# Kernel tuning notes

Measured on AMD Instinct MI355X. Metric: run time of the kernel, lower is better.

Reference implementation:

```python
import jax, jax.numpy as jnp
import numpy as np

NDIV = (10, 10)
OUT_CHANNEL = 100


def setup_inputs() -> dict:
    key = jax.random.key(0)
    k1, k2 = jax.random.split(key)
    x1 = jax.random.normal(k1, (8, 64, 128, 128), dtype=jnp.float32)
    x2 = jax.random.normal(k2, (8, 64, 60, 60), dtype=jnp.float32)
    return {"x1": x1, "x2": x2}


def reference(x1, x2):
    B, C, H, W = x1.shape
    h, w = x2.shape[-2], x2.shape[-1]
    nd0, nd1 = NDIV
    hh, ww = h // nd0, w // nd1  # patch size (6, 6)
    P = nd0 * nd1                # 100 patches per sample

    # channel-wise L2 normalization (dim=1)
    x1n = x1 / jnp.linalg.norm(x1, axis=1, keepdims=True)
    x2n = x2 / jnp.linalg.norm(x2, axis=1, keepdims=True)

    # extract nd0*nd1 patches per sample as conv filters: [B*P, C, hh, ww]
    patches = x2n.reshape(B, C, nd0, hh, nd1, ww)
    patches = patches.transpose(0, 2, 4, 1, 3, 5).reshape(B * P, C, hh, ww)

    # grouped cross-correlation (torch F.conv2d = correlation, no kernel flip)
    lhs = x1n.reshape(1, B * C, H, W)
    mm = jax.lax.conv_general_dilated(
        lhs, patches,
        window_strides=(1, 1),
        padding=((hh // 2, hh // 2), (ww // 2, ww // 2)),
        feature_group_count=B,
        dimension_numbers=("NCHW", "OIHW", "NCHW"),
    ) / (hh * ww)  # [1, B*P, H+1, W+1] for even hh,ww

    # bilinear resize to (H, W)  (torch align_corners=False == half-pixel)
    mm = jax.image.resize(mm, (1, B * P, H, W), method="bilinear")

    # [B, P, H, W] -> topk over patch dim, then mean
    mm = mm.reshape(B, P, H, W)
    topv = jax.lax.top_k(jnp.moveaxis(mm, 1, -1), OUT_CHANNEL)[0]  # [B,H,W,k]
    out = jnp.mean(topv, axis=-1)[:, None]  # [B,1,H,W]
    return out
```

## Files before the change

kernel.cpp:

```cpp
#include <hip/hip_runtime.h>
#include <cstddef>

#define BB   8
#define CC   64
#define H1   128
#define W1   128
#define HW1  (H1*W1)
#define HS   60
#define WS   60
#define HO   129
#define WO   129

#define PWD  144
#define PHT  134
#define PPL  (PHT*PWD)

#define G     16
#define CPG   4
#define T4    19
#define TROWS 70
#define NSLOT (TROWS*T4)
#define PSTR  132
#define PPLANE (HO*PSTR)

typedef unsigned int u32;
__device__ __forceinline__ void async_g2l(const float* g, float4* l) {
    __builtin_amdgcn_global_load_lds((const __attribute__((address_space(1))) u32*)g,
                                     (__attribute__((address_space(3))) u32*)l,
                                     16, 0, 0);
}

__global__ __launch_bounds__(256) void k_norm1(const float* __restrict__ x1,
                                               float* __restrict__ x1n) {
    int idx = blockIdx.x * 256 + threadIdx.x;
    int b  = idx / PPL;
    int pp = idx - b * PPL;
    int pr = pp / PWD, pc = pp - pr * PWD;
    int gy = pr - 3, gx = pc - 3;
    float* outp = x1n + (size_t)b * CC * PPL + pp;
    if ((unsigned)gy < 128u && (unsigned)gx < 128u) {
        const float* p = x1 + (size_t)b * CC * HW1 + gy * W1 + gx;
        float v[CC];
        float s = 0.f;
#pragma unroll
        for (int c = 0; c < CC; ++c) { v[c] = p[c * HW1]; s += v[c] * v[c]; }
        float inv = 1.0f / sqrtf(s);
#pragma unroll
        for (int c = 0; c < CC; ++c) outp[c * PPL] = v[c] * inv;
    } else {
#pragma unroll
        for (int c = 0; c < CC; ++c) outp[c * PPL] = 0.f;
    }
}

__global__ __launch_bounds__(256) void k_inv2(const float* __restrict__ x2,
                                              float* __restrict__ inv2) {
    __shared__ float red[256];
    int tid = threadIdx.x;
    int pix = blockIdx.x * 64 + (tid & 63);
    int csub = tid >> 6;
    int b  = pix / (HS * WS);
    int hw = pix % (HS * WS);
    const float* p = x2 + ((size_t)b * CC + csub * 16) * (HS * WS) + hw;
    float s = 0.f;
#pragma unroll
    for (int c = 0; c < 16; ++c) {
        float v = p[c * (HS * WS)];
        s += v * v;
    }
    red[tid] = s;
    __syncthreads();
    if (tid < 64) {
        float t = red[tid] + red[tid + 64] + red[tid + 128] + red[tid + 192];
        inv2[blockIdx.x * 64 + tid] = 1.0f / sqrtf(t);
    }
}

__global__ __launch_bounds__(256) void k_fold(const float* __restrict__ x2,
                                              const float* __restrict__ inv2,
                                              float* __restrict__ S) {
    __shared__ float bins[36];
    int tid = threadIdx.x;
    int bc  = blockIdx.x;
    int b   = bc >> 6;
    if (tid < 36) bins[tid] = 0.f;
    __syncthreads();
    const float* px = x2 + (size_t)bc * (HS * WS);
    const float* pn = inv2 + b * (HS * WS);
    for (int i = tid; i < HS * WS; i += 256) {
        int hh = i / WS, ww = i - hh * WS;
        int bin = (hh % 6) * 6 + (ww % 6);
        atomicAdd(&bins[bin], px[i] * pn[i]);
    }
    __syncthreads();
    if (tid < 36) S[bc * 36 + tid] = bins[tid];
}

__global__ __launch_bounds__(256) void k_conv(const float* __restrict__ x1n,
                                              const float* __restrict__ S,
                                              float* __restrict__ part) {
    int blk = blockIdx.x;
    int x0 = (blk & 1) * 64;
    int y0 = ((blk >> 1) & 1) * 64;
    int b  = (blk >> 2) & 7;
    int g  = blk >> 5;
    int tid = threadIdx.x;
    int tx = tid & 15, ty = tid >> 4;
    int wv = tid >> 6;

    __shared__ float4 lbuf[2][NSLOT];
    __shared__ float4 svf[CPG][9];

    if (tid < CPG * 36)
        ((float*)svf)[tid] = S[((size_t)b * CC + g * CPG) * 36 + tid];

    int off[6];
#pragma unroll
    for (int k = 0; k < 6; ++k) {
        int i = tid + 256 * k;
        int r = i / T4, c4 = i - r * T4;
        off[k] = (y0 + r) * PWD + x0 + 4 * c4;
    }

    const float* gbase = x1n + ((size_t)b * CC + g * CPG) * PPL;

#pragma unroll
    for (int k = 0; k < 5; ++k)
        async_g2l(gbase + off[k], &lbuf[0][wv * 64 + 256 * k]);
    if (tid < NSLOT - 1280)
        async_g2l(gbase + off[5], &lbuf[0][wv * 64 + 1280]);

    float acc[4][5] = {{0,0,0,0,0},{0,0,0,0,0},{0,0,0,0,0},{0,0,0,0,0}};
    float accE[5] = {0,0,0,0,0};
    const bool doC4 = (x0 == 64) && (tx == 15);
    const bool doR4 = (y0 == 64) && (ty == 15);

    for (int ci = 0; ci < CPG; ++ci) {
        __syncthreads();

        if (ci + 1 < CPG) {
            const float* gp = gbase + (size_t)(ci + 1) * PPL;
            float4* dst = lbuf[(ci + 1) & 1];
#pragma unroll
            for (int k = 0; k < 5; ++k)
                async_g2l(gp + off[k], &dst[wv * 64 + 256 * k]);
            if (tid < NSLOT - 1280)
                async_g2l(gp + off[5], &dst[wv * 64 + 1280]);
        }

        float s[36];
        const float4* sp = (const float4*)svf[ci];
#pragma unroll
        for (int t = 0; t < 9; ++t) {
            float4 w = sp[t];
            s[4*t] = w.x; s[4*t+1] = w.y; s[4*t+2] = w.z; s[4*t+3] = w.w;
        }

        const float4* tb = lbuf[ci & 1];
#pragma unroll
        for (int rr = 0; rr < 9; ++rr) {
            const float4* rp = tb + (4 * ty + rr) * T4 + tx;
            float4 q0 = rp[0], q1 = rp[1], q2 = rp[2];
            float r[12] = {q0.x,q0.y,q0.z,q0.w, q1.x,q1.y,q1.z,q1.w,
                           q2.x,q2.y,q2.z,q2.w};
#pragma unroll
            for (int q = 0; q < 4; ++q) {
                int dy = rr - q;
                if (dy >= 0 && dy < 6) {
#pragma unroll
                    for (int j = 0; j < 4; ++j)
#pragma unroll
                        for (int dx = 0; dx < 6; ++dx)
                            acc[q][j] += r[j + dx] * s[dy * 6 + dx];
                    if (doC4) {
#pragma unroll
                        for (int dx = 0; dx < 6; ++dx)
                            acc[q][4] += r[4 + dx] * s[dy * 6 + dx];
                    }
                }
            }
            if (doR4 && rr >= 4) {
                int dy = rr - 4;
#pragma unroll
                for (int j = 0; j < 4; ++j)
#pragma unroll
                    for (int dx = 0; dx < 6; ++dx)
                        accE[j] += r[j + dx] * s[dy * 6 + dx];
                if (doC4) {
#pragma unroll
                    for (int dx = 0; dx < 6; ++dx)
                        accE[4] += r[4 + dx] * s[dy * 6 + dx];
                }
            }
        }
        if (doR4) {
            const float4* rp = tb + (4 * ty + 9) * T4 + tx;
            float4 q0 = rp[0], q1 = rp[1], q2 = rp[2];
            float r[12] = {q0.x,q0.y,q0.z,q0.w, q1.x,q1.y,q1.z,q1.w,
                           q2.x,q2.y,q2.z,q2.w};
#pragma unroll
            for (int j = 0; j < 4; ++j)
#pragma unroll
                for (int dx = 0; dx < 6; ++dx)
                    accE[j] += r[j + dx] * s[30 + dx];
            if (doC4) {
#pragma unroll
                for (int dx = 0; dx < 6; ++dx)
                    accE[4] += r[4 + dx] * s[30 + dx];
            }
        }
    }

    float* pb = part + ((size_t)g * BB + b) * PPLANE;
    int orow = y0 + 4 * ty, ocol = x0 + 4 * tx;
#pragma unroll
    for (int q = 0; q < 4; ++q)
        *(float4*)(pb + (size_t)(orow + q) * PSTR + ocol) =
            make_float4(acc[q][0], acc[q][1], acc[q][2], acc[q][3]);
    if (doC4) {
#pragma unroll
        for (int q = 0; q < 4; ++q)
            pb[(size_t)(orow + q) * PSTR + 128] = acc[q][4];
    }
    if (doR4) {
        *(float4*)(pb + (size_t)128 * PSTR + ocol) =
            make_float4(accE[0], accE[1], accE[2], accE[3]);
        if (doC4) pb[(size_t)128 * PSTR + 128] = accE[4];
    }
}

__global__ __launch_bounds__(256) void k_reduce(const float* __restrict__ part,
                                                float* __restrict__ out129) {
    int idx = blockIdx.x * 256 + threadIdx.x;
    if (idx >= BB * HO * WO) return;
    int b = idx / (HO * WO);
    int p = idx % (HO * WO);
    int row = p / WO, col = p - row * WO;
    float s = 0.f;
#pragma unroll
    for (int g = 0; g < G; ++g)
        s += part[((size_t)g * BB + b) * PPLANE + (size_t)row * PSTR + col];
    out129[idx] = s * (1.0f / 3600.0f);
}

__global__ __launch_bounds__(256) void k_resize(const float* __restrict__ out129,
                                                float* __restrict__ out) {
    int idx = blockIdx.x * 256 + threadIdx.x;
    int b  = idx >> 14;
    int oy = (idx >> 7) & 127;
    int ox = idx & 127;

    const float inv_scale = 129.0f / 128.0f;
    const float ksc       = 128.0f / 129.0f;

    float sy = (oy + 0.5f) * inv_scale - 0.5f;
    float sx = (ox + 0.5f) * inv_scale - 0.5f;
    int fy = (int)floorf(sy);
    int fx = (int)floorf(sx);

    float wy[4], wx[4];
    float sumy = 0.f, sumx = 0.f;
#pragma unroll
    for (int k = 0; k < 4; ++k) {
        int jy = fy - 1 + k;
        float w = 0.f;
        if (jy >= 0 && jy < HO) w = fmaxf(0.f, 1.0f - fabsf(sy - (float)jy) * ksc);
        wy[k] = w; sumy += w;
        int jx = fx - 1 + k;
        float w2 = 0.f;
        if (jx >= 0 && jx < WO) w2 = fmaxf(0.f, 1.0f - fabsf(sx - (float)jx) * ksc);
        wx[k] = w2; sumx += w2;
    }

    const float* p = out129 + (size_t)b * (HO * WO);
    float r = 0.f;
#pragma unroll
    for (int ky = 0; ky < 4; ++ky) {
        if (wy[ky] == 0.f) continue;
        int jy = fy - 1 + ky;
        float rowv = 0.f;
#pragma unroll
        for (int kx = 0; kx < 4; ++kx) {
            if (wx[kx] == 0.f) continue;
            rowv += wx[kx] * p[jy * WO + (fx - 1 + kx)];
        }
        r += wy[ky] * rowv;
    }
    out[idx] = r / (sumy * sumx);
}

extern "C" void kernel_launch(void* const* d_in, const int* in_sizes, int n_in,
                              void* d_out, int out_size, void* d_ws, size_t ws_size,
                              hipStream_t stream) {
    const float* x1 = (const float*)d_in[0];
    const float* x2 = (const float*)d_in[1];
    float* out = (float*)d_out;

    float* ws     = (float*)d_ws;
    float* inv2   = ws;
    float* Sbuf   = inv2 + BB * HS * WS;
    float* x1n    = Sbuf + BB * CC * 36;
    float* part   = x1n + (size_t)BB * CC * PPL;
    float* out129 = part + (size_t)G * BB * PPLANE;

    k_norm1 <<<(BB * PPL) / 256, 256, 0, stream>>>(x1, x1n);
    k_inv2  <<<(BB * HS * WS) / 64, 256, 0, stream>>>(x2, inv2);
    k_fold  <<<BB * CC, 256, 0, stream>>>(x2, inv2, Sbuf);
    k_conv  <<<4 * BB * G, 256, 0, stream>>>(x1n, Sbuf, part);
    k_reduce<<<(BB * HO * WO + 255) / 256, 256, 0, stream>>>(part, out129);
    k_resize<<<(BB * HW1) / 256, 256, 0, stream>>>(out129, out);
}
```

Before: 140.6 us.

## Fuse six kernels into three: prep, conv, and reduce+resize output

Merges the x1 normalization, x2 inverse-norm and patch fold into one launch, with x2 norm computed per chunk and written as per-chunk partial sums that the conv kernel reduces while loading filters. The group-partial reduction and the bilinear resize are fused into one tiled kernel that stages a 36x36 reduced tile in shared memory and writes float4 outputs. This removes three launches and the out129 round trip through global memory and avoids LDS atomics in the fold. The cost is redundant reduction of halo pixels in the output kernel and only 128 blocks for that stage.

```diff
diff --git a/kernel.cpp b/kernel.cpp
--- a/kernel.cpp
+++ b/kernel.cpp
@@ -23,6 +23,10 @@
 #define PSTR  132
 #define PPLANE (HO*PSTR)
 
+#define NCHUNK 15
+#define NBLK_NORM 603
+#define NBLK_PRE  (BB*NCHUNK)
+
 typedef unsigned int u32;
 __device__ __forceinline__ void async_g2l(const float* g, float4* l) {
     __builtin_amdgcn_global_load_lds((const __attribute__((address_space(1))) u32*)g,
@@ -30,74 +34,70 @@
                                      16, 0, 0);
 }
 
-__global__ __launch_bounds__(256) void k_norm1(const float* __restrict__ x1,
-                                               float* __restrict__ x1n) {
-    int idx = blockIdx.x * 256 + threadIdx.x;
-    int b  = idx / PPL;
-    int pp = idx - b * PPL;
-    int pr = pp / PWD, pc = pp - pr * PWD;
-    int gy = pr - 3, gx = pc - 3;
-    float* outp = x1n + (size_t)b * CC * PPL + pp;
-    if ((unsigned)gy < 128u && (unsigned)gx < 128u) {
-        const float* p = x1 + (size_t)b * CC * HW1 + gy * W1 + gx;
-        float v[CC];
-        float s = 0.f;
-#pragma unroll
-        for (int c = 0; c < CC; ++c) { v[c] = p[c * HW1]; s += v[c] * v[c]; }
-        float inv = 1.0f / sqrtf(s);
-#pragma unroll
-        for (int c = 0; c < CC; ++c) outp[c * PPL] = v[c] * inv;
+__global__ __launch_bounds__(256) void k_prep(const float* __restrict__ x1,
+                                              const float* __restrict__ x2,
+                                              float* __restrict__ x1n,
+                                              float* __restrict__ Spart) {
+    __shared__ float inv[240];
+    int tid = threadIdx.x;
+
+    if (blockIdx.x < NBLK_NORM) {
+        int idx = blockIdx.x * 256 + tid;
+        int b  = idx / PPL;
+        int pp = idx - b * PPL;
+        int pr = pp / PWD, pc = pp - pr * PWD;
+        int gy = pr - 3, gx = pc - 3;
+        float* outp = x1n + (size_t)b * CC * PPL + pp;
+        if ((unsigned)gy < 128u && (unsigned)gx < 128u) {
+            const float* p = x1 + (size_t)b * CC * HW1 + gy * W1 + gx;
+            float v[CC];
+            float s = 0.f;
+#pragma unroll
+            for (int c = 0; c < CC; ++c) { v[c] = p[c * HW1]; s += v[c] * v[c]; }
+            float iv = 1.0f / sqrtf(s);
+#pragma unroll
+            for (int c = 0; c < CC; ++c) outp[c * PPL] = v[c] * iv;
+        } else {
+#pragma unroll
+            for (int c = 0; c < CC; ++c) outp[c * PPL] = 0.f;
+        }
     } else {
-#pragma unroll
-        for (int c = 0; c < CC; ++c) outp[c * PPL] = 0.f;
-    }
-}
-
-__global__ __launch_bounds__(256) void k_inv2(const float* __restrict__ x2,
-                                              float* __restrict__ inv2) {
-    __shared__ float red[256];
-    int tid = threadIdx.x;
-    int pix = blockIdx.x * 64 + (tid & 63);
-    int csub = tid >> 6;
-    int b  = pix / (HS * WS);
-    int hw = pix % (HS * WS);
-    const float* p = x2 + ((size_t)b * CC + csub * 16) * (HS * WS) + hw;
-    float s = 0.f;
-#pragma unroll
-    for (int c = 0; c < 16; ++c) {
-        float v = p[c * (HS * WS)];
-        s += v * v;
-    }
-    red[tid] = s;
-    __syncthreads();
-    if (tid < 64) {
-        float t = red[tid] + red[tid + 64] + red[tid + 128] + red[tid + 192];
-        inv2[blockIdx.x * 64 + tid] = 1.0f / sqrtf(t);
-    }
-}
-
-__global__ __launch_bounds__(256) void k_fold(const float* __restrict__ x2,
-                                              const float* __restrict__ inv2,
-                                              float* __restrict__ S) {
-    __shared__ float bins[36];
-    int tid = threadIdx.x;
-    int bc  = blockIdx.x;
-    int b   = bc >> 6;
-    if (tid < 36) bins[tid] = 0.f;
-    __syncthreads();
-    const float* px = x2 + (size_t)bc * (HS * WS);
-    const float* pn = inv2 + b * (HS * WS);
-    for (int i = tid; i < HS * WS; i += 256) {
-        int hh = i / WS, ww = i - hh * WS;
-        int bin = (hh % 6) * 6 + (ww % 6);
-        atomicAdd(&bins[bin], px[i] * pn[i]);
-    }
-    __syncthreads();
-    if (tid < 36) S[bc * 36 + tid] = bins[tid];
+        int pb = blockIdx.x - NBLK_NORM;
+        int b = pb / NCHUNK, chunk = pb - b * NCHUNK;
+        int px0 = chunk * 240;
+
+        if (tid < 240) {
+            const float* p = x2 + (size_t)b * CC * (HS * WS) + px0 + tid;
+            float s = 0.f;
+#pragma unroll
+            for (int c = 0; c < CC; ++c) { float v = p[c * (HS * WS)]; s += v * v; }
+            inv[tid] = 1.0f / sqrtf(s);
+        }
+        __syncthreads();
+
+        int c = tid >> 2, q = tid & 3;
+        int row = chunk * 4 + q;
+        const float* px = x2 + ((size_t)b * CC + c) * (HS * WS) + row * WS;
+        const float* iv = inv + q * 60;
+        float acc[6] = {0, 0, 0, 0, 0, 0};
+#pragma unroll
+        for (int i = 0; i < 60; ++i)
+            acc[i % 6] += px[i] * iv[i];
+
+        float* sb = Spart + (((size_t)b * CC + c) * NCHUNK + chunk) * 36;
+        int r0 = row % 6;
+#pragma unroll
+        for (int j = 0; j < 6; ++j) sb[r0 * 6 + j] = acc[j];
+        if (q < 2) {
+            int rm = (chunk * 4 + 4 + q) % 6;
+#pragma unroll
+            for (int j = 0; j < 6; ++j) sb[rm * 6 + j] = 0.f;
+        }
+    }
 }
 
 __global__ __launch_bounds__(256) void k_conv(const float* __restrict__ x1n,
-                                              const float* __restrict__ S,
+                                              const float* __restrict__ Spart,
                                               float* __restrict__ part) {
     int blk = blockIdx.x;
     int x0 = (blk & 1) * 64;
@@ -111,8 +111,14 @@
     __shared__ float4 lbuf[2][NSLOT];
     __shared__ float4 svf[CPG][9];
 
-    if (tid < CPG * 36)
-        ((float*)svf)[tid] = S[((size_t)b * CC + g * CPG) * 36 + tid];
+    if (tid < CPG * 36) {
+        int ci = tid / 36, bin = tid - ci * 36;
+        const float* sp = Spart + (((size_t)b * CC + g * CPG + ci) * NCHUNK) * 36 + bin;
+        float s = 0.f;
+#pragma unroll
+        for (int k = 0; k < NCHUNK; ++k) s += sp[k * 36];
+        ((float*)svf)[tid] = s;
+    }
 
     int off[6];
 #pragma unroll
@@ -229,64 +235,80 @@
     }
 }
 
-__global__ __launch_bounds__(256) void k_reduce(const float* __restrict__ part,
-                                                float* __restrict__ out129) {
-    int idx = blockIdx.x * 256 + threadIdx.x;
-    if (idx >= BB * HO * WO) return;
-    int b = idx / (HO * WO);
-    int p = idx % (HO * WO);
-    int row = p / WO, col = p - row * WO;
-    float s = 0.f;
-#pragma unroll
-    for (int g = 0; g < G; ++g)
-        s += part[((size_t)g * BB + b) * PPLANE + (size_t)row * PSTR + col];
-    out129[idx] = s * (1.0f / 3600.0f);
-}
-
-__global__ __launch_bounds__(256) void k_resize(const float* __restrict__ out129,
-                                                float* __restrict__ out) {
-    int idx = blockIdx.x * 256 + threadIdx.x;
-    int b  = idx >> 14;
-    int oy = (idx >> 7) & 127;
-    int ox = idx & 127;
+__global__ __launch_bounds__(256) void k_out(const float* __restrict__ part,
+                                             float* __restrict__ out) {
+    __shared__ float m[36 * 37];
+    int blk  = blockIdx.x;
+    int b    = blk >> 4;
+    int tile = blk & 15;
+    int oy0 = (tile >> 2) * 32, ox0 = (tile & 3) * 32;
+    int tid = threadIdx.x;
+    int ry0 = oy0 - 1, rx0 = ox0 - 1;
+
+    for (int i = tid; i < 36 * 36; i += 256) {
+        int ly = i / 36, lx = i - ly * 36;
+        int jy = min(max(ry0 + ly, 0), 128);
+        int jx = min(max(rx0 + lx, 0), 128);
+        const float* pp = part + (size_t)b * PPLANE + jy * PSTR + jx;
+        float s = 0.f;
+#pragma unroll
+        for (int g = 0; g < G; ++g) s += pp[(size_t)g * BB * PPLANE];
+        m[ly * 37 + lx] = s * (1.0f / 3600.0f);
+    }
+    __syncthreads();
 
     const float inv_scale = 129.0f / 128.0f;
     const float ksc       = 128.0f / 129.0f;
 
+    int oy  = oy0 + (tid >> 3);
+    int oxb = ox0 + (tid & 7) * 4;
+
     float sy = (oy + 0.5f) * inv_scale - 0.5f;
-    float sx = (ox + 0.5f) * inv_scale - 0.5f;
     int fy = (int)floorf(sy);
-    int fx = (int)floorf(sx);
-
-    float wy[4], wx[4];
-    float sumy = 0.f, sumx = 0.f;
+    float wy[4];
+    float sumy = 0.f;
 #pragma unroll
     for (int k = 0; k < 4; ++k) {
         int jy = fy - 1 + k;
         float w = 0.f;
         if (jy >= 0 && jy < HO) w = fmaxf(0.f, 1.0f - fabsf(sy - (float)jy) * ksc);
         wy[k] = w; sumy += w;
-        int jx = fx - 1 + k;
-        float w2 = 0.f;
-        if (jx >= 0 && jx < WO) w2 = fmaxf(0.f, 1.0f - fabsf(sx - (float)jx) * ksc);
-        wx[k] = w2; sumx += w2;
-    }
-
-    const float* p = out129 + (size_t)b * (HO * WO);
-    float r = 0.f;
-#pragma unroll
-    for (int ky = 0; ky < 4; ++ky) {
-        if (wy[ky] == 0.f) continue;
-        int jy = fy - 1 + ky;
-        float rowv = 0.f;
-#pragma unroll
-        for (int kx = 0; kx < 4; ++kx) {
-            if (wx[kx] == 0.f) continue;
-            rowv += wx[kx] * p[jy * WO + (fx - 1 + kx)];
-        }
-        r += wy[ky] * rowv;
-    }
-    out[idx] = r / (sumy * sumx);
+    }
+
+    float res[4];
+#pragma unroll
+    for (int j = 0; j < 4; ++j) {
+        int ox = oxb + j;
+        float sx = (ox + 0.5f) * inv_scale - 0.5f;
+        int fx = (int)floorf(sx);
+        float wx[4];
+        float sumx = 0.f;
+#pragma unroll
+        for (int k = 0; k < 4; ++k) {
+            int jx = fx - 1 + k;
+            float w = 0.f;
+            if (jx >= 0 && jx < WO) w = fmaxf(0.f, 1.0f - fabsf(sx - (float)jx) * ksc);
+            wx[k] = w; sumx += w;
+        }
+        float r = 0.f;
+#pragma unroll
+        for (int ky = 0; ky < 4; ++ky) {
+            if (wy[ky] == 0.f) continue;
+            int ly = fy - 1 + ky - ry0;
+            float rowv = 0.f;
+#pragma unroll
+            for (int kx = 0; kx < 4; ++kx) {
+                if (wx[kx] == 0.f) continue;
+                int lx = fx - 1 + kx - rx0;
+                rowv += wx[kx] * m[ly * 37 + lx];
+            }
+            r += wy[ky] * rowv;
+        }
+        res[j] = r / (sumy * sumx);
+    }
+
+    *(float4*)(out + (size_t)b * HW1 + oy * W1 + oxb) =
+        make_float4(res[0], res[1], res[2], res[3]);
 }
 
 extern "C" void kernel_launch(void* const* d_in, const int* in_sizes, int n_in,
@@ -296,17 +318,12 @@
     const float* x2 = (const float*)d_in[1];
     float* out = (float*)d_out;
 
-    float* ws     = (float*)d_ws;
-    float* inv2   = ws;
-    float* Sbuf   = inv2 + BB * HS * WS;
-    float* x1n    = Sbuf + BB * CC * 36;
-    float* part   = x1n + (size_t)BB * CC * PPL;
-    float* out129 = part + (size_t)G * BB * PPLANE;
-
-    k_norm1 <<<(BB * PPL) / 256, 256, 0, stream>>>(x1, x1n);
-    k_inv2  <<<(BB * HS * WS) / 64, 256, 0, stream>>>(x2, inv2);
-    k_fold  <<<BB * CC, 256, 0, stream>>>(x2, inv2, Sbuf);
-    k_conv  <<<4 * BB * G, 256, 0, stream>>>(x1n, Sbuf, part);
-    k_reduce<<<(BB * HO * WO + 255) / 256, 256, 0, stream>>>(part, out129);
-    k_resize<<<(BB * HW1) / 256, 256, 0, stream>>>(out129, out);
-}
+    float* ws    = (float*)d_ws;
+    float* x1n   = ws;
+    float* part  = x1n + (size_t)BB * CC * PPL;
+    float* Spart = part + (size_t)G * BB * PPLANE;
+
+    k_prep<<<NBLK_NORM + NBLK_PRE, 256, 0, stream>>>(x1, x2, x1n, Spart);
+    k_conv<<<4 * BB * G, 256, 0, stream>>>(x1n, Spart, part);
+    k_out <<<BB * 16, 256, 0, stream>>>(part, out);
+}
```

After: 137.4 us. -2.3%, faster.
